# Kernel tuning notes

Measured on AMD Instinct MI355X. Metric: run time of the kernel, lower is better.

## Reference

```python
import jax, jax.numpy as jnp
import numpy as np

P = 2  # lrtd_pad (p_l == p_r == p_t == p_d)
B, C, H, W = 4, 64, 128, 128


def setup_inputs() -> dict:
    key = jax.random.key(0)
    x = jax.random.normal(key, (B, 6, C, H, W), dtype=jnp.float32)
    return {"x": x}


def _cube_pad(x):
    # faces: [B,C,H,W] each; order matches torch module unpacking
    fb, fd, ff, fl, fr, ft = (x[:, i] for i in range(6))
    flip_h = lambda a: a[:, :, ::-1, :]   # flip along dim 2 (rows)
    flip_w = lambda a: a[:, :, :, ::-1]   # flip along dim 3 (cols)
    T = lambda a: jnp.swapaxes(a, 2, 3)   # permute(0,1,3,2)

    # top strips for faces 0..5 -> [B,6,C,P,W]
    top = jnp.stack([
        flip_h(ft[:, :, :P, :]),           # back
        ff[:, :, -P:, :],                  # down
        ft[:, :, -P:, :],                  # front
        T(ft[:, :, :, :P]),                # left
        flip_h(T(ft[:, :, :, -P:])),       # right
        flip_h(fb[:, :, :P, :]),           # top
    ], axis=1)

    # bottom strips -> [B,6,C,P,W]
    bot = jnp.stack([
        flip_h(fd[:, :, -P:, :]),
        flip_h(fb[:, :, -P:, :]),
        fd[:, :, :P, :],
        flip_h(T(fd[:, :, :, :P])),
        T(fd[:, :, :, -P:]),
        ff[:, :, :P, :],
    ], axis=1)

    # left strips -> [B,6,C,H,P]
    lft = jnp.stack([
        fr[:, :, :, -P:],
        flip_w(T(fl[:, :, -P:, :])),
        fl[:, :, :, -P:],
        fb[:, :, :, -P:],
        ff[:, :, :, -P:],
        T(fl[:, :, :P, :]),
    ], axis=1)

    # right strips -> [B,6,C,H,P]
    rgt = jnp.stack([
        fl[:, :, :, :P],
        T(fr[:, :, -P:, :]),
        fr[:, :, :, :P],
        ff[:, :, :, :P],
        fb[:, :, :, :P],
        flip_w(T(fr[:, :, :P, :])),
    ], axis=1)

    # corners: equal pads -> repeat the top/bottom strip's edge column along width
    p_tl = jnp.tile(top[:, :, :, :P, :1], (1, 1, 1, 1, P))
    p_tr = jnp.tile(top[:, :, :, -P:, -1:], (1, 1, 1, 1, P))
    p_dl = jnp.tile(bot[:, :, :, :P, :1], (1, 1, 1, 1, P))
    p_dr = jnp.tile(bot[:, :, :, -P:, -1:], (1, 1, 1, 1, P))

    mid = jnp.concatenate([top, x, bot], axis=3)            # [B,6,C,H+2P,W]
    left = jnp.concatenate([p_tl, lft, p_dl], axis=3)       # [B,6,C,H+2P,P]
    right = jnp.concatenate([p_tr, rgt, p_dr], axis=3)      # [B,6,C,H+2P,P]
    return jnp.concatenate([left, mid, right], axis=4)      # [B,6,C,H+2P,W+2P]


def reference(x):
    return _cube_pad(x)
```

## Files before the change

### kernel.cpp

```cpp
#include <hip/hip_runtime.h>


typedef float f32x4 __attribute__((ext_vector_type(4)));
typedef f32x4 f32x4_a8 __attribute__((aligned(8)));

constexpr int P = 2, B = 4, C = 64, H = 128, W = 128;
constexpr int Ho = H + 2 * P, Wo = W + 2 * P;
constexpr int NV = Wo / 4;
constexpr int PLANES = B * 6 * C;
constexpr int ROWS   = PLANES * H;

constexpr int BLK_EDGE = ROWS / 256;
constexpr int NHALO    = PLANES * 4 * NV;
constexpr int BLK_HALO = NHALO / 256;
constexpr int BLK_A    = ROWS * 32 / 256;
constexpr int BLK_B    = BLK_EDGE + BLK_HALO;
constexpr int BLOCKS   = BLK_B + BLK_A;

__device__ __forceinline__ void top_map(int f, int t, int w, int& sf, int& r, int& col) {
    switch (f) {
        case 0:  sf = 5; r = P - 1 - t; col = w;         break;
        case 1:  sf = 2; r = H - P + t; col = w;         break;
        case 2:  sf = 5; r = H - P + t; col = w;         break;
        case 3:  sf = 5; r = w;         col = t;         break;
        case 4:  sf = 5; r = w;         col = W - 1 - t; break;
        default: sf = 0; r = P - 1 - t; col = w;         break;
    }
}
__device__ __forceinline__ void bot_map(int f, int t, int w, int& sf, int& r, int& col) {
    switch (f) {
        case 0:  sf = 1; r = H - 1 - t; col = w;         break;
        case 1:  sf = 0; r = H - 1 - t; col = w;         break;
        case 2:  sf = 1; r = t;         col = w;         break;
        case 3:  sf = 1; r = w;         col = P - 1 - t; break;
        case 4:  sf = 1; r = w;         col = W - P + t; break;
        default: sf = 2; r = t;         col = w;         break;
    }
}
__device__ __forceinline__ void lft_map(int f, int h, int l, int& sf, int& r, int& col) {
    switch (f) {
        case 0:  sf = 4; r = h;         col = W - P + l; break;
        case 1:  sf = 3; r = H - 1 - l; col = h;         break;
        case 2:  sf = 3; r = h;         col = W - P + l; break;
        case 3:  sf = 0; r = h;         col = W - P + l; break;
        case 4:  sf = 2; r = h;         col = W - P + l; break;
        default: sf = 3; r = l;         col = h;         break;
    }
}
__device__ __forceinline__ void rgt_map(int f, int h, int rr, int& sf, int& r, int& col) {
    switch (f) {
        case 0:  sf = 3; r = h;          col = rr;        break;
        case 1:  sf = 4; r = H - P + rr; col = h;         break;
        case 2:  sf = 4; r = h;          col = rr;        break;
        case 3:  sf = 2; r = h;          col = rr;        break;
        case 4:  sf = 0; r = h;          col = rr;        break;
        default: sf = 4; r = P - 1 - rr; col = h;         break;
    }
}

__device__ __forceinline__ void gen_map(int f, int i, int j, int& sf, int& r, int& col) {
    bool in_h = (i >= P) && (i < H + P);
    bool in_w = (j >= P) && (j < W + P);
    if (in_h && in_w) {
        sf = f; r = i - P; col = j - P;
    } else if (!in_h) {
        int w = in_w ? (j - P) : (j < P ? 0 : W - 1);
        if (i < P) top_map(f, i, w, sf, r, col);
        else       bot_map(f, i - H - P, w, sf, r, col);
    } else {
        if (j < P) lft_map(f, i - P, j,         sf, r, col);
        else       rgt_map(f, i - P, j - W - P, sf, r, col);
    }
}

__global__ __launch_bounds__(256) void cubepad_v8_kernel(const float* __restrict__ x,
                                                         float* __restrict__ out) {
    const int bid = blockIdx.x;
    const int tid = threadIdx.x;

    if (bid >= BLK_B) {
        const unsigned idx = (unsigned)(bid - BLK_B) * 256u + (unsigned)tid;
        const unsigned g   = idx & 31u;
        const unsigned row = idx >> 5;
        const unsigned i   = row & (unsigned)(H - 1);
        const unsigned p   = row >> 7;

        const f32x4 v = *(const f32x4*)(x + ((size_t)row << 7) + (g << 2));

        const size_t o = (size_t)p * (Ho * Wo) + (size_t)(i + P) * Wo + (g << 2) + P;
        __builtin_nontemporal_store(v, (f32x4_a8*)(out + o));
        return;
    }

    if (bid < BLK_EDGE) {
        const unsigned row = (unsigned)bid * 256u + (unsigned)tid;
        const unsigned i   = row & (unsigned)(H - 1);
        const unsigned p   = row >> 7;
        const int f  = (int)((p >> 6) % 6u);
        const int bC = (int)(((p >> 6) / 6u) * (6u * C) + (p & 63u));

        int sf, r, col;
        float2 lv, rv;
        lft_map(f, (int)i, 0, sf, r, col);
        lv.x = x[((size_t)(bC + sf * C)) * (H * W) + ((size_t)r << 7) + col];
        lft_map(f, (int)i, 1, sf, r, col);
        lv.y = x[((size_t)(bC + sf * C)) * (H * W) + ((size_t)r << 7) + col];
        rgt_map(f, (int)i, 0, sf, r, col);
        rv.x = x[((size_t)(bC + sf * C)) * (H * W) + ((size_t)r << 7) + col];
        rgt_map(f, (int)i, 1, sf, r, col);
        rv.y = x[((size_t)(bC + sf * C)) * (H * W) + ((size_t)r << 7) + col];

        const size_t rb = (size_t)p * (Ho * Wo) + (size_t)(i + P) * Wo;
        *(float2*)(out + rb)            = lv;
        *(float2*)(out + rb + (W + P))  = rv;
        return;
    }

    const unsigned h = (unsigned)(bid - BLK_EDGE) * 256u + (unsigned)tid;
    const unsigned v    = h % (unsigned)NV;
    const unsigned t2   = h / (unsigned)NV;
    const unsigned t    = t2 & 3u;
    const unsigned p    = t2 >> 2;
    const int i_out = (t < 2u) ? (int)t : (H + P + (int)t - 2);
    const int f  = (int)((p >> 6) % 6u);
    const int bC = (int)(((p >> 6) / 6u) * (6u * C) + (p & 63u));

    f32x4 val;
    #pragma unroll
    for (int e = 0; e < 4; ++e) {
        int sf, r, col;
        gen_map(f, i_out, (int)(4u * v) + e, sf, r, col);
        val[e] = x[((size_t)(bC + sf * C)) * (H * W) + ((size_t)r << 7) + col];
    }
    const size_t o = (size_t)p * (Ho * Wo) + (size_t)i_out * Wo + ((size_t)v << 2);
    __builtin_nontemporal_store(val, (f32x4*)(out + o));
}

extern "C" void kernel_launch(void* const* d_in, const int* in_sizes, int n_in,
                              void* d_out, int out_size, void* d_ws, size_t ws_size,
                              hipStream_t stream) {
    const float* x = (const float*)d_in[0];
    float* out = (float*)d_out;
    cubepad_v8_kernel<<<BLOCKS, 256, 0, stream>>>(x, out);
}
```

Baseline: 193.2 us.

## Stage 8-row bands in LDS to emit full aligned padded rows

Replaces the separate interior-copy blocks and left/right edge blocks with band blocks. Each band block loads 8 input rows into shared memory and writes complete output rows, including edge columns, as 16-byte-aligned float4 stores. The old interior stores were misaligned by the 2-column pad and the edge writes were separate float2 stores. The change adds a barrier, an LDS round trip, a divide by 33, and some lane imbalance, since 264 work items are spread over 256 threads.

```diff
diff --git a/kernel.cpp b/kernel.cpp
--- a/kernel.cpp
+++ b/kernel.cpp
@@ -8,14 +8,11 @@
 constexpr int Ho = H + 2 * P, Wo = W + 2 * P;
 constexpr int NV = Wo / 4;
 constexpr int PLANES = B * 6 * C;
-constexpr int ROWS   = PLANES * H;
 
-constexpr int BLK_EDGE = ROWS / 256;
 constexpr int NHALO    = PLANES * 4 * NV;
 constexpr int BLK_HALO = NHALO / 256;
-constexpr int BLK_A    = ROWS * 32 / 256;
-constexpr int BLK_B    = BLK_EDGE + BLK_HALO;
-constexpr int BLOCKS   = BLK_B + BLK_A;
+constexpr int BANDS    = PLANES * (H / 8);
+constexpr int BLOCKS   = BLK_HALO + BANDS;
 
 __device__ __forceinline__ void top_map(int f, int t, int w, int& sf, int& r, int& col) {
     switch (f) {
@@ -73,54 +70,63 @@
     }
 }
 
-__global__ __launch_bounds__(256) void cubepad_v8_kernel(const float* __restrict__ x,
-                                                         float* __restrict__ out) {
+__global__ __launch_bounds__(256) void cubepad_v10_kernel(const float* __restrict__ x,
+                                                          float* __restrict__ out) {
+    __shared__ float lds[8 * W];
     const int bid = blockIdx.x;
     const int tid = threadIdx.x;
 
-    if (bid >= BLK_B) {
-        const unsigned idx = (unsigned)(bid - BLK_B) * 256u + (unsigned)tid;
-        const unsigned g   = idx & 31u;
-        const unsigned row = idx >> 5;
-        const unsigned i   = row & (unsigned)(H - 1);
-        const unsigned p   = row >> 7;
+    if (bid >= BLK_HALO) {
+        const int band = bid - BLK_HALO;
+        const int p    = band >> 4;
+        const int r0   = (band & 15) << 3;
+        const int f    = (p >> 6) % 6;
+        const int bC   = ((p >> 6) / 6) * (6 * C) + (p & 63);
+        const float* plane = x + (size_t)p * (H * W);
 
-        const f32x4 v = *(const f32x4*)(x + ((size_t)row << 7) + (g << 2));
+        {
+            const int r = tid >> 5, g = tid & 31;
+            const f32x4 v = *(const f32x4*)(plane + ((size_t)(r0 + r) << 7) + (g << 2));
+            *(f32x4*)(&lds[tid << 2]) = v;
+        }
+        __syncthreads();
 
-        const size_t o = (size_t)p * (Ho * Wo) + (size_t)(i + P) * Wo + (g << 2) + P;
-        __builtin_nontemporal_store(v, (f32x4_a8*)(out + o));
+        const size_t ob = (size_t)p * (Ho * Wo);
+        for (int m = tid; m < 8 * NV; m += 256) {
+            const unsigned r = (unsigned)m / 33u;
+            const int g = m - (int)(r * 33u);
+            const int i = r0 + (int)r;
+            f32x4 o;
+            if (g == 0) {
+                int sf, rr, cc;
+                lft_map(f, i, 0, sf, rr, cc);
+                o[0] = x[((size_t)(bC + sf * C)) * (H * W) + ((size_t)rr << 7) + cc];
+                lft_map(f, i, 1, sf, rr, cc);
+                o[1] = x[((size_t)(bC + sf * C)) * (H * W) + ((size_t)rr << 7) + cc];
+                o[2] = lds[(r << 7) + 0];
+                o[3] = lds[(r << 7) + 1];
+            } else if (g == NV - 1) {
+                o[0] = lds[(r << 7) + 126];
+                o[1] = lds[(r << 7) + 127];
+                int sf, rr, cc;
+                rgt_map(f, i, 0, sf, rr, cc);
+                o[2] = x[((size_t)(bC + sf * C)) * (H * W) + ((size_t)rr << 7) + cc];
+                rgt_map(f, i, 1, sf, rr, cc);
+                o[3] = x[((size_t)(bC + sf * C)) * (H * W) + ((size_t)rr << 7) + cc];
+            } else {
+                o = *(const f32x4_a8*)(&lds[(r << 7) + (g << 2) - 2]);
+            }
+            __builtin_nontemporal_store(
+                o, (f32x4*)(out + ob + (size_t)(i + P) * Wo + ((size_t)g << 2)));
+        }
         return;
     }
 
-    if (bid < BLK_EDGE) {
-        const unsigned row = (unsigned)bid * 256u + (unsigned)tid;
-        const unsigned i   = row & (unsigned)(H - 1);
-        const unsigned p   = row >> 7;
-        const int f  = (int)((p >> 6) % 6u);
-        const int bC = (int)(((p >> 6) / 6u) * (6u * C) + (p & 63u));
-
-        int sf, r, col;
-        float2 lv, rv;
-        lft_map(f, (int)i, 0, sf, r, col);
-        lv.x = x[((size_t)(bC + sf * C)) * (H * W) + ((size_t)r << 7) + col];
-        lft_map(f, (int)i, 1, sf, r, col);
-        lv.y = x[((size_t)(bC + sf * C)) * (H * W) + ((size_t)r << 7) + col];
-        rgt_map(f, (int)i, 0, sf, r, col);
-        rv.x = x[((size_t)(bC + sf * C)) * (H * W) + ((size_t)r << 7) + col];
-        rgt_map(f, (int)i, 1, sf, r, col);
-        rv.y = x[((size_t)(bC + sf * C)) * (H * W) + ((size_t)r << 7) + col];
-
-        const size_t rb = (size_t)p * (Ho * Wo) + (size_t)(i + P) * Wo;
-        *(float2*)(out + rb)            = lv;
-        *(float2*)(out + rb + (W + P))  = rv;
-        return;
-    }
-
-    const unsigned h = (unsigned)(bid - BLK_EDGE) * 256u + (unsigned)tid;
-    const unsigned v    = h % (unsigned)NV;
-    const unsigned t2   = h / (unsigned)NV;
-    const unsigned t    = t2 & 3u;
-    const unsigned p    = t2 >> 2;
+    const unsigned h  = (unsigned)bid * 256u + (unsigned)tid;
+    const unsigned v  = h % (unsigned)NV;
+    const unsigned t2 = h / (unsigned)NV;
+    const unsigned t  = t2 & 3u;
+    const unsigned p  = t2 >> 2;
     const int i_out = (t < 2u) ? (int)t : (H + P + (int)t - 2);
     const int f  = (int)((p >> 6) % 6u);
     const int bC = (int)(((p >> 6) / 6u) * (6u * C) + (p & 63u));
@@ -141,5 +147,5 @@
                               hipStream_t stream) {
     const float* x = (const float*)d_in[0];
     float* out = (float*)d_out;
-    cubepad_v8_kernel<<<BLOCKS, 256, 0, stream>>>(x, out);
+    cubepad_v10_kernel<<<BLOCKS, 256, 0, stream>>>(x, out);
 }
```

Result: faster. 186.5 us (-3.5%).
